# Kernel optimization log

Hardware: AMD Instinct MI355X
Metric: run time of the kernel (lower is better)

Reference implementation:

```python
import jax, jax.numpy as jnp
import numpy as np

V, D, H, KVH, HD, I, L, T_MAX, THETA = 32000, 1024, 16, 4, 64, 2816, 2, 2048, 10000.0
EPS = 1e-5


def rmsnorm(x, w):
    return x * jax.lax.rsqrt(jnp.mean(x * x, axis=-1, keepdims=True) + EPS) * w


def rope_cos_sin(T):
    inv = 1.0 / (THETA ** (jnp.arange(0, HD, 2, dtype=jnp.float32) / HD))  # [HD/2]
    ang = jnp.arange(T, dtype=jnp.float32)[:, None] * inv[None, :]         # [T, HD/2]
    return jnp.cos(ang), jnp.sin(ang)


def apply_rope(x, cos, sin):
    # x: [B, T, h, HD]; interleaved complex pairs as in torch.view_as_complex
    x0 = x[..., 0::2]
    x1 = x[..., 1::2]
    c = cos[None, :, None, :]
    s = sin[None, :, None, :]
    o0 = x0 * c - x1 * s
    o1 = x0 * s + x1 * c
    return jnp.stack([o0, o1], axis=-1).reshape(x.shape)


def setup_inputs() -> dict:
    key = jax.random.key(0)
    ks = jax.random.split(key, 12)
    sc = 0.02
    return {
        "toks": jax.random.randint(ks[0], (1, 2048), 0, V),
        "embed": jax.random.normal(ks[1], (V, D), jnp.float32) * sc,
        "Wq": jax.random.normal(ks[2], (L, D, H * HD), jnp.float32) * sc,
        "Wk": jax.random.normal(ks[3], (L, D, KVH * HD), jnp.float32) * sc,
        "Wv": jax.random.normal(ks[4], (L, D, KVH * HD), jnp.float32) * sc,
        "Wo": jax.random.normal(ks[5], (L, H * HD, D), jnp.float32) * sc,
        "Wgate": jax.random.normal(ks[6], (L, D, I), jnp.float32) * sc,
        "Wup": jax.random.normal(ks[7], (L, D, I), jnp.float32) * sc,
        "Wdown": jax.random.normal(ks[8], (L, I, D), jnp.float32) * sc,
        "ln1_w": jnp.ones((L, D), jnp.float32),
        "ln2_w": jnp.ones((L, D), jnp.float32),
        "norm_w": jnp.ones((D,), jnp.float32),
        "Wlm": jax.random.normal(ks[9], (D, V), jnp.float32) * sc,
    }


def reference(toks, embed, Wq, Wk, Wv, Wo, Wgate, Wup, Wdown, ln1_w, ln2_w, norm_w, Wlm):
    B, T = toks.shape
    cos, sin = rope_cos_sin(T)
    causal = jnp.tril(jnp.ones((T, T), dtype=bool))
    add_mask = jnp.where(causal, 0.0, -jnp.inf).astype(jnp.float32)  # [T, T]
    n_rep = H // KVH
    scale = 1.0 / np.sqrt(HD)

    x = embed[toks]  # [B, T, D]
    for l in range(L):
        h = rmsnorm(x, ln1_w[l])
        q = (h @ Wq[l]).reshape(B, T, H, HD)
        k = (h @ Wk[l]).reshape(B, T, KVH, HD)
        v = (h @ Wv[l]).reshape(B, T, KVH, HD)
        q = apply_rope(q, cos, sin)
        k = apply_rope(k, cos, sin)
        k = jnp.repeat(k, n_rep, axis=2)  # GQA repeat_kv -> [B, T, H, HD]
        v = jnp.repeat(v, n_rep, axis=2)
        # materialized scores [B, H, T, T] (faithful to source)
        scores = jnp.einsum('bqhd,bkhd->bhqk', q, k) * scale + add_mask[None, None]
        probs = jax.nn.softmax(scores, axis=-1)
        attn = jnp.einsum('bhqk,bkhd->bqhd', probs, v).reshape(B, T, H * HD)
        x = x + attn @ Wo[l]
        h = rmsnorm(x, ln2_w[l])
        x = x + (jax.nn.silu(h @ Wgate[l]) * (h @ Wup[l])) @ Wdown[l]

    x = rmsnorm(x, norm_w)
    return x @ Wlm  # [B, T, V]
```

## Files before the change

### kernel.cpp

```cpp
#include <hip/hip_runtime.h>

#define T_SEQ 2048
#define DMODEL 1024
#define NH 16
#define NKV 4
#define HEAD_DIM 64
#define FFDIM 2816
#define NVOCAB 32000

#define QBLK 64
#define KBLK 128
#define KSS 72
#define VTS 136
#define PSS 136

using u16 = unsigned short;
typedef __bf16 bf16x8 __attribute__((ext_vector_type(8)));
typedef float f32x4 __attribute__((ext_vector_type(4)));

__device__ __forceinline__ float b2f(u16 u) {
    union { unsigned int i; float f; } v; v.i = ((unsigned int)u) << 16; return v.f;
}
__device__ __forceinline__ u16 f2b(float f) {
    unsigned int u = __builtin_bit_cast(unsigned int, f);
    unsigned int r = (u + 0x7FFFu + ((u >> 16) & 1u)) >> 16;
    return (u16)r;
}
__device__ __forceinline__ void gload16(const u16* g, u16* l) {
    __builtin_amdgcn_global_load_lds(
        (const __attribute__((address_space(1))) void*)g,
        (__attribute__((address_space(3))) void*)l, 16, 0, 0);
}

__global__ __launch_bounds__(256) void embed_kernel(const int* __restrict__ toks,
                                                    const float* __restrict__ emb,
                                                    float* __restrict__ x) {
    int idx = blockIdx.x * 256 + threadIdx.x;
    int t = idx >> 10, d = idx & 1023;
    x[idx] = emb[(size_t)toks[t] * DMODEL + d];
}

__global__ __launch_bounds__(256) void rmsnorm_kernel(const float* __restrict__ x,
                                                      const float* __restrict__ w,
                                                      u16* __restrict__ out) {
    __shared__ float red[256];
    const int row = blockIdx.x, tid = threadIdx.x;
    const float* xr = x + (size_t)row * DMODEL;
    float vals[4]; float ss = 0.f;
#pragma unroll
    for (int i = 0; i < 4; i++) { float v = xr[tid + 256 * i]; vals[i] = v; ss += v * v; }
    red[tid] = ss; __syncthreads();
    for (int s = 128; s > 0; s >>= 1) { if (tid < s) red[tid] += red[tid + s]; __syncthreads(); }
    float inv = rsqrtf(red[0] * (1.0f / DMODEL) + 1e-5f);
#pragma unroll
    for (int i = 0; i < 4; i++) {
        int c = tid + 256 * i;
        out[(size_t)row * DMODEL + c] = f2b(vals[i] * inv * w[c]);
    }
}

__global__ __launch_bounds__(256) void tcast_kernel(const float* __restrict__ in,
                                                    u16* __restrict__ out, int K, int N) {
    __shared__ float tile[32][33];
    int bx = blockIdx.x * 32;
    int by = blockIdx.y * 32;
    int tx = threadIdx.x & 31, ty = threadIdx.x >> 5;
#pragma unroll
    for (int i = 0; i < 32; i += 8)
        tile[ty + i][tx] = in[(size_t)(by + ty + i) * N + bx + tx];
    __syncthreads();
#pragma unroll
    for (int i = 0; i < 32; i += 8)
        out[(size_t)(bx + ty + i) * K + by + tx] = f2b(tile[tx][ty + i]);
}

__global__ __launch_bounds__(256) void vtcast_kernel(const float* __restrict__ fqkv,
                                                     u16* __restrict__ vt) {
    __shared__ float tile[32][33];
    int bx = blockIdx.x * 32;
    int by = blockIdx.y * 32;
    int tx = threadIdx.x & 31, ty = threadIdx.x >> 5;
#pragma unroll
    for (int i = 0; i < 32; i += 8)
        tile[ty + i][tx] = fqkv[(size_t)(by + ty + i) * 1536 + 1280 + bx + tx];
    __syncthreads();
#pragma unroll
    for (int i = 0; i < 32; i += 8)
        vt[(size_t)(bx + ty + i) * T_SEQ + by + tx] = f2b(tile[tx][ty + i]);
}

__global__ __launch_bounds__(256) void gemm_bt_kernel(const u16* __restrict__ A,
                                                      const u16* __restrict__ BT,
                                                      float* __restrict__ C,
                                                      int N, int K) {
    __shared__ __align__(16) u16 As[128 * 32];
    __shared__ __align__(16) u16 Bs[128 * 32];
    const int tid = threadIdx.x;
    const int brow = blockIdx.x, bcol = blockIdx.y;
    const int w = tid >> 6, lane = tid & 63;
    const int wr = w >> 1, wc = w & 1;
    const int lg = lane >> 4, lr = lane & 15;

    f32x4 acc[4][4] = {};

    const int srow = w * 32 + (lane >> 2);
    const int scol = (lane & 3) << 3;
    const u16* gA = A + (size_t)(brow * 128 + srow) * K + scol;
    const u16* gB = BT + (size_t)(bcol * 128 + srow) * K + scol;
    u16* lA0 = &As[(w * 32) * 32];
    u16* lA1 = &As[(w * 32 + 16) * 32];
    u16* lB0 = &Bs[(w * 32) * 32];
    u16* lB1 = &Bs[(w * 32 + 16) * 32];

    for (int kb = 0; kb < K; kb += 32) {
        gload16(gA + kb, lA0);
        gload16(gA + (size_t)16 * K + kb, lA1);
        gload16(gB + kb, lB0);
        gload16(gB + (size_t)16 * K + kb, lB1);
        __syncthreads();

        bf16x8 aF[4], bF[4];
#pragma unroll
        for (int m = 0; m < 4; m++)
            aF[m] = *(const bf16x8*)(&As[(wr * 64 + m * 16 + lr) * 32 + lg * 8]);
#pragma unroll
        for (int n = 0; n < 4; n++)
            bF[n] = *(const bf16x8*)(&Bs[(wc * 64 + n * 16 + lr) * 32 + lg * 8]);
#pragma unroll
        for (int m = 0; m < 4; m++)
#pragma unroll
            for (int n = 0; n < 4; n++)
                acc[m][n] = __builtin_amdgcn_mfma_f32_16x16x32_bf16(aF[m], bF[n], acc[m][n], 0, 0, 0);
        __syncthreads();
    }

#pragma unroll
    for (int m = 0; m < 4; m++)
#pragma unroll
        for (int n = 0; n < 4; n++)
#pragma unroll
            for (int j = 0; j < 4; j++) {
                int row = brow * 128 + wr * 64 + m * 16 + lg * 4 + j;
                int col = bcol * 128 + wc * 64 + n * 16 + lr;
                C[(size_t)row * N + col] = acc[m][n][j];
            }
}

__device__ __forceinline__ int bs_off(int c, int k) {
    return c * 40 + ((((k >> 3) ^ ((c >> 3) & 3)) << 3) | (k & 7));
}

__global__ __launch_bounds__(256) void gemm_f32b_kernel(const u16* __restrict__ A,
                                                        const float* __restrict__ B,
                                                        float* __restrict__ C,
                                                        int N, int K) {
    __shared__ __align__(16) u16 As[128 * 40];
    __shared__ __align__(16) u16 Bs[128 * 40];
    const int tid = threadIdx.x;
    const int brow = blockIdx.y, bcol = blockIdx.x;
    const int wid = tid >> 6, lane = tid & 63;
    const int wr = wid >> 1, wc = wid & 1;
    const int lg = lane >> 4, lr = lane & 15;

    f32x4 acc[4][4] = {};
    const int ar = tid >> 2, ac = (tid & 3) << 3;
    const int bk = tid >> 4, bc = (tid & 15) << 3;

    for (int kb = 0; kb < K; kb += 32) {
        {
            const u16* ga = A + (size_t)(brow * 128 + ar) * K + kb + ac;
            *(uint4*)(&As[ar * 40 + ac]) = *(const uint4*)ga;
            *(uint4*)(&As[(ar + 64) * 40 + ac]) = *(const uint4*)(ga + (size_t)64 * K);
        }
        {
            const float* gb = B + (size_t)(kb + bk) * N + bcol * 128 + bc;
            float4 a0 = *(const float4*)gb;
            float4 a1 = *(const float4*)(gb + 4);
            float4 b0 = *(const float4*)(gb + (size_t)16 * N);
            float4 b1 = *(const float4*)(gb + (size_t)16 * N + 4);
            float f0[8] = {a0.x, a0.y, a0.z, a0.w, a1.x, a1.y, a1.z, a1.w};
            float f1[8] = {b0.x, b0.y, b0.z, b0.w, b1.x, b1.y, b1.z, b1.w};
#pragma unroll
            for (int i = 0; i < 8; i++) {
                Bs[bs_off(bc + i, bk)] = f2b(f0[i]);
                Bs[bs_off(bc + i, bk + 16)] = f2b(f1[i]);
            }
        }
        __syncthreads();

        bf16x8 aF[4], bF[4];
#pragma unroll
        for (int m = 0; m < 4; m++)
            aF[m] = *(const bf16x8*)(&As[(wr * 64 + m * 16 + lr) * 40 + lg * 8]);
#pragma unroll
        for (int n = 0; n < 4; n++) {
            int c = wc * 64 + n * 16 + lr;
            bF[n] = *(const bf16x8*)(&Bs[c * 40 + ((lg ^ ((c >> 3) & 3)) << 3)]);
        }
#pragma unroll
        for (int m = 0; m < 4; m++)
#pragma unroll
            for (int n = 0; n < 4; n++)
                acc[m][n] = __builtin_amdgcn_mfma_f32_16x16x32_bf16(aF[m], bF[n], acc[m][n], 0, 0, 0);
        __syncthreads();
    }

#pragma unroll
    for (int m = 0; m < 4; m++)
#pragma unroll
        for (int n = 0; n < 4; n++)
#pragma unroll
            for (int j = 0; j < 4; j++) {
                int row = brow * 128 + wr * 64 + m * 16 + lg * 4 + j;
                int col = bcol * 128 + wc * 64 + n * 16 + lr;
                C[(size_t)row * N + col] = acc[m][n][j];
            }
}

__global__ __launch_bounds__(256) void rope_kernel(const float* __restrict__ in,
                                                   u16* __restrict__ out, int heads,
                                                   int instride, int incoloff) {
    int idx = blockIdx.x * 256 + threadIdx.x;
    int total = T_SEQ * heads * 32;
    if (idx >= total) return;
    int i = idx & 31;
    int rest = idx >> 5;
    int t = rest / heads, hh = rest - t * heads;
    float inv = expf(-(float)i * (9.210340371976184f / 32.0f));
    float ang = (float)t * inv;
    float c = cosf(ang), s = sinf(ang);
    size_t src = (size_t)t * instride + incoloff + hh * HEAD_DIM + 2 * i;
    size_t dst = (size_t)rest * HEAD_DIM + 2 * i;
    float x0 = in[src], x1 = in[src + 1];
    out[dst]     = f2b(x0 * c - x1 * s);
    out[dst + 1] = f2b(x0 * s + x1 * c);
}

__global__ __launch_bounds__(256) void fattn_kernel(const u16* __restrict__ q,
                                                    const u16* __restrict__ k,
                                                    const u16* __restrict__ vt,
                                                    u16* __restrict__ out) {
    __shared__ __align__(16) u16 Ks[KBLK * KSS];
    __shared__ __align__(16) u16 Vt[HEAD_DIM * VTS];
    __shared__ __align__(16) u16 Ps[QBLK * PSS];
    const int tid = threadIdx.x;
    const int qb0 = blockIdx.x * QBLK, h = blockIdx.y, kvh = h >> 2;
    const int w = tid >> 6, lane = tid & 63;
    const int lg = lane >> 4, lr = lane & 15;

    bf16x8 qf0, qf1;
    {
        const u16* src = q + ((size_t)(qb0 + w * 16 + lr) * NH + h) * HEAD_DIM;
        qf0 = *(const bf16x8*)(src + lg * 8);
        qf1 = *(const bf16x8*)(src + 32 + lg * 8);
    }

    f32x4 acc_o[4] = {};
    float m_run[4] = {-1e30f, -1e30f, -1e30f, -1e30f};
    float l_run[4] = {0.f, 0.f, 0.f, 0.f};

    const int ntiles = (qb0 + QBLK - 1) / KBLK + 1;

    for (int kt = 0; kt < ntiles; kt++) {
        const int kb = kt * KBLK;
        __syncthreads();
        for (int c = tid; c < KBLK * 8; c += 256) {
            int row = c >> 3, c8 = (c & 7) << 3;
            *(uint4*)(&Ks[row * KSS + c8]) =
                *(const uint4*)(k + ((size_t)(kb + row) * NKV + kvh) * HEAD_DIM + c8);
        }
        for (int c = tid; c < HEAD_DIM * 16; c += 256) {
            int d = c >> 4, c16 = (c & 15) << 3;
            *(uint4*)(&Vt[d * VTS + c16]) =
                *(const uint4*)(vt + (size_t)(kvh * HEAD_DIM + d) * T_SEQ + kb + c16);
        }
        __syncthreads();

        f32x4 s[8] = {};
#pragma unroll
        for (int n = 0; n < 8; n++) {
            bf16x8 kf0 = *(const bf16x8*)(&Ks[(n * 16 + lr) * KSS + lg * 8]);
            bf16x8 kf1 = *(const bf16x8*)(&Ks[(n * 16 + lr) * KSS + 32 + lg * 8]);
            s[n] = __builtin_amdgcn_mfma_f32_16x16x32_bf16(qf0, kf0, s[n], 0, 0, 0);
            s[n] = __builtin_amdgcn_mfma_f32_16x16x32_bf16(qf1, kf1, s[n], 0, 0, 0);
        }

#pragma unroll
        for (int j = 0; j < 4; j++) {
            int q_g = qb0 + w * 16 + lg * 4 + j;
            float sv[8];
            float tmax = -1e30f;
#pragma unroll
            for (int n = 0; n < 8; n++) {
                float xx = s[n][j] * 0.125f;
                if (kb + n * 16 + lr > q_g) xx = -1e30f;
                sv[n] = xx;
                tmax = fmaxf(tmax, xx);
            }
#pragma unroll
            for (int mm = 1; mm < 16; mm <<= 1) tmax = fmaxf(tmax, __shfl_xor(tmax, mm));
            float mn = fmaxf(m_run[j], tmax);
            float sc = __expf(m_run[j] - mn);
            m_run[j] = mn;
            float rsum = 0.f;
#pragma unroll
            for (int n = 0; n < 8; n++) {
                float p = __expf(sv[n] - mn);
                rsum += p;
                Ps[(w * 16 + lg * 4 + j) * PSS + n * 16 + lr] = f2b(p);
            }
#pragma unroll
            for (int mm = 1; mm < 16; mm <<= 1) rsum += __shfl_xor(rsum, mm);
            l_run[j] = l_run[j] * sc + rsum;
#pragma unroll
            for (int n = 0; n < 4; n++) acc_o[n][j] *= sc;
        }

#pragma unroll
        for (int ks = 0; ks < 4; ks++) {
            bf16x8 pf = *(const bf16x8*)(&Ps[(w * 16 + lr) * PSS + ks * 32 + lg * 8]);
#pragma unroll
            for (int n = 0; n < 4; n++) {
                bf16x8 vf = *(const bf16x8*)(&Vt[(n * 16 + lr) * VTS + ks * 32 + lg * 8]);
                acc_o[n] = __builtin_amdgcn_mfma_f32_16x16x32_bf16(pf, vf, acc_o[n], 0, 0, 0);
            }
        }
    }

#pragma unroll
    for (int n = 0; n < 4; n++)
#pragma unroll
        for (int j = 0; j < 4; j++) {
            int t = qb0 + w * 16 + lg * 4 + j;
            int d = n * 16 + lr;
            out[((size_t)t * NH + h) * HEAD_DIM + d] = f2b(acc_o[n][j] / l_run[j]);
        }
}

__global__ __launch_bounds__(256) void silu_mul_kernel(const float* __restrict__ gu,
                                                       u16* __restrict__ out) {
    int t = blockIdx.x;
    int c = blockIdx.y * 256 + threadIdx.x;
    float gv = gu[(size_t)t * 5632 + c];
    float uv = gu[(size_t)t * 5632 + 2816 + c];
    float s = gv / (1.f + __expf(-gv));
    out[(size_t)t * FFDIM + c] = f2b(s * uv);
}

__global__ __launch_bounds__(256) void add_kernel(float* __restrict__ x,
                                                  const float* __restrict__ y, int n) {
    int i = blockIdx.x * 256 + threadIdx.x;
    if (i < n) x[i] += y[i];
}

extern "C" void kernel_launch(void* const* d_in, const int* in_sizes, int n_in,
                              void* d_out, int out_size, void* d_ws, size_t ws_size,
                              hipStream_t stream) {
    const int*   toks = (const int*)d_in[0];
    const float* emb  = (const float*)d_in[1];
    const float* Wq   = (const float*)d_in[2];
    const float* Wk   = (const float*)d_in[3];
    const float* Wv   = (const float*)d_in[4];
    const float* Wo   = (const float*)d_in[5];
    const float* Wg   = (const float*)d_in[6];
    const float* Wu   = (const float*)d_in[7];
    const float* Wd   = (const float*)d_in[8];
    const float* ln1  = (const float*)d_in[9];
    const float* ln2  = (const float*)d_in[10];
    const float* nw   = (const float*)d_in[11];
    const float* Wlm  = (const float*)d_in[12];

    char* ob = (char*)d_out;
    const size_t MB = 1024 * 1024;
    float* x    = (float*)(ob + 0 * MB);
    float* fqkv = (float*)(ob + 8 * MB);
    float* fGU  = (float*)(ob + 20 * MB);
    float* fA   = (float*)(ob + 64 * MB);
    u16* vt     = (u16*)  (ob + 72 * MB);
    u16* qb     = (u16*)  (ob + 74 * MB);
    u16* kb     = (u16*)  (ob + 78 * MB);
    u16* attnb  = (u16*)  (ob + 80 * MB);
    u16* ffb    = (u16*)  (ob + 84 * MB);
    size_t woff = 96 * MB;
    auto walloc = [&](size_t elems) {
        u16* p = (u16*)(ob + woff);
        woff += ((elems * 2 + 255) & ~(size_t)255);
        return p;
    };
    u16 *WqkvT[2], *WoT[2], *WguT[2], *WdT[2];
    for (int l = 0; l < 2; l++) {
        WqkvT[l] = walloc((size_t)1536 * DMODEL);
        WoT[l]   = walloc((size_t)DMODEL * DMODEL);
        WguT[l]  = walloc((size_t)5632 * DMODEL);
        WdT[l]   = walloc((size_t)DMODEL * FFDIM);
    }
    u16* h = (u16*)d_ws;
    bool ws_big = ws_size >= 72 * MB;
    u16* WlmT = ws_big ? (u16*)((char*)d_ws + 4 * MB) : nullptr;
    (void)in_sizes; (void)n_in; (void)out_size;

    dim3 blk(256);
    auto tcast = [&](const float* in, u16* out, int K, int N) {
        tcast_kernel<<<dim3(N / 32, K / 32), blk, 0, stream>>>(in, out, K, N);
    };
    auto gemm_bt = [&](const u16* A, const u16* BT, float* C, int N, int K) {
        dim3 g(T_SEQ / 128, N / 128);
        gemm_bt_kernel<<<g, blk, 0, stream>>>(A, BT, C, N, K);
    };

    for (int l = 0; l < 2; l++) {
        tcast(Wq + (size_t)l * DMODEL * NH * HEAD_DIM,  WqkvT[l],                    DMODEL, NH * HEAD_DIM);
        tcast(Wk + (size_t)l * DMODEL * NKV * HEAD_DIM, WqkvT[l] + (size_t)1024 * DMODEL, DMODEL, NKV * HEAD_DIM);
        tcast(Wv + (size_t)l * DMODEL * NKV * HEAD_DIM, WqkvT[l] + (size_t)1280 * DMODEL, DMODEL, NKV * HEAD_DIM);
        tcast(Wo + (size_t)l * DMODEL * DMODEL,         WoT[l],  DMODEL, DMODEL);
        tcast(Wg + (size_t)l * DMODEL * FFDIM,          WguT[l],                     DMODEL, FFDIM);
        tcast(Wu + (size_t)l * DMODEL * FFDIM,          WguT[l] + (size_t)FFDIM * DMODEL, DMODEL, FFDIM);
        tcast(Wd + (size_t)l * FFDIM * DMODEL,          WdT[l],  FFDIM, DMODEL);
    }
    if (WlmT) tcast(Wlm, WlmT, DMODEL, NVOCAB);

    embed_kernel<<<dim3(T_SEQ * DMODEL / 256), blk, 0, stream>>>(toks, emb, x);

    for (int l = 0; l < 2; l++) {
        rmsnorm_kernel<<<dim3(T_SEQ), blk, 0, stream>>>(x, ln1 + (size_t)l * DMODEL, h);
        gemm_bt(h, WqkvT[l], fqkv, 1536, DMODEL);
        rope_kernel<<<dim3(T_SEQ * NH * 32 / 256), blk, 0, stream>>>(fqkv, qb, NH, 1536, 0);
        rope_kernel<<<dim3(T_SEQ * NKV * 32 / 256), blk, 0, stream>>>(fqkv, kb, NKV, 1536, 1024);
        vtcast_kernel<<<dim3(8, T_SEQ / 32), blk, 0, stream>>>(fqkv, vt);
        fattn_kernel<<<dim3(T_SEQ / QBLK, NH), blk, 0, stream>>>(qb, kb, vt, attnb);
        gemm_bt(attnb, WoT[l], fA, DMODEL, DMODEL);
        add_kernel<<<dim3(T_SEQ * DMODEL / 256), blk, 0, stream>>>(x, fA, T_SEQ * DMODEL);

        rmsnorm_kernel<<<dim3(T_SEQ), blk, 0, stream>>>(x, ln2 + (size_t)l * DMODEL, h);
        gemm_bt(h, WguT[l], fGU, 5632, DMODEL);
        silu_mul_kernel<<<dim3(T_SEQ, FFDIM / 256), blk, 0, stream>>>(fGU, ffb);
        gemm_bt(ffb, WdT[l], fA, DMODEL, FFDIM);
        add_kernel<<<dim3(T_SEQ * DMODEL / 256), blk, 0, stream>>>(x, fA, T_SEQ * DMODEL);
    }

    rmsnorm_kernel<<<dim3(T_SEQ), blk, 0, stream>>>(x, nw, h);
    if (WlmT) {
        gemm_bt(h, WlmT, (float*)d_out, NVOCAB, DMODEL);
    } else {
        dim3 g(NVOCAB / 128, T_SEQ / 128);
        gemm_f32b_kernel<<<g, blk, 0, stream>>>(h, Wlm, (float*)d_out, NVOCAB, DMODEL);
    }
}
```

Before: 906.9 us.

## Double-buffer LDS tiles and remap workgroups across XCDs in bf16 GEMM

Converts the GEMM K-loop to double-buffered LDS so the next tile's global-to-LDS load is issued before computing on the current tile, leaving one barrier per iteration. Also remaps the linear workgroup id so consecutive tiles run on the same XCD, improving L2 reuse of A/B rows. This doubles LDS use per block, which may lower occupancy, and relies on the async loads finishing before the single barrier.

```diff
diff --git a/kernel.cpp b/kernel.cpp
--- a/kernel.cpp
+++ b/kernel.cpp
@@ -93,10 +93,17 @@
                                                       const u16* __restrict__ BT,
                                                       float* __restrict__ C,
                                                       int N, int K) {
-    __shared__ __align__(16) u16 As[128 * 32];
-    __shared__ __align__(16) u16 Bs[128 * 32];
+    __shared__ __align__(16) u16 As[2][128 * 32];
+    __shared__ __align__(16) u16 Bs[2][128 * 32];
     const int tid = threadIdx.x;
-    const int brow = blockIdx.x, bcol = blockIdx.y;
+    const int gx = gridDim.x;
+    const int nwg = gx * gridDim.y;
+    const int hwid = blockIdx.y * gx + blockIdx.x;
+    const int q = nwg >> 3, r = nwg & 7;
+    const int xcd = hwid & 7, rem = hwid >> 3;
+    const int wgid = (xcd < r ? xcd * (q + 1) : r * (q + 1) + (xcd - r) * q) + rem;
+    const int brow = wgid % gx, bcol = wgid / gx;
+
     const int w = tid >> 6, lane = tid & 63;
     const int wr = w >> 1, wc = w & 1;
     const int lg = lane >> 4, lr = lane & 15;
@@ -107,31 +114,39 @@
     const int scol = (lane & 3) << 3;
     const u16* gA = A + (size_t)(brow * 128 + srow) * K + scol;
     const u16* gB = BT + (size_t)(bcol * 128 + srow) * K + scol;
-    u16* lA0 = &As[(w * 32) * 32];
-    u16* lA1 = &As[(w * 32 + 16) * 32];
-    u16* lB0 = &Bs[(w * 32) * 32];
-    u16* lB1 = &Bs[(w * 32 + 16) * 32];
-
-    for (int kb = 0; kb < K; kb += 32) {
-        gload16(gA + kb, lA0);
-        gload16(gA + (size_t)16 * K + kb, lA1);
-        gload16(gB + kb, lB0);
-        gload16(gB + (size_t)16 * K + kb, lB1);
-        __syncthreads();
-
+    const int lofs0 = (w * 32) * 32;
+    const int lofs1 = (w * 32 + 16) * 32;
+
+    const int nt = K >> 5;
+    gload16(gA, &As[0][lofs0]);
+    gload16(gA + (size_t)16 * K, &As[0][lofs1]);
+    gload16(gB, &Bs[0][lofs0]);
+    gload16(gB + (size_t)16 * K, &Bs[0][lofs1]);
+    __syncthreads();
+
+    int cur = 0;
+    for (int t = 0; t < nt; t++) {
+        if (t + 1 < nt) {
+            const int kb = (t + 1) << 5;
+            gload16(gA + kb, &As[cur ^ 1][lofs0]);
+            gload16(gA + (size_t)16 * K + kb, &As[cur ^ 1][lofs1]);
+            gload16(gB + kb, &Bs[cur ^ 1][lofs0]);
+            gload16(gB + (size_t)16 * K + kb, &Bs[cur ^ 1][lofs1]);
+        }
         bf16x8 aF[4], bF[4];
 #pragma unroll
         for (int m = 0; m < 4; m++)
-            aF[m] = *(const bf16x8*)(&As[(wr * 64 + m * 16 + lr) * 32 + lg * 8]);
+            aF[m] = *(const bf16x8*)(&As[cur][(wr * 64 + m * 16 + lr) * 32 + lg * 8]);
 #pragma unroll
         for (int n = 0; n < 4; n++)
-            bF[n] = *(const bf16x8*)(&Bs[(wc * 64 + n * 16 + lr) * 32 + lg * 8]);
+            bF[n] = *(const bf16x8*)(&Bs[cur][(wc * 64 + n * 16 + lr) * 32 + lg * 8]);
 #pragma unroll
         for (int m = 0; m < 4; m++)
 #pragma unroll
             for (int n = 0; n < 4; n++)
                 acc[m][n] = __builtin_amdgcn_mfma_f32_16x16x32_bf16(aF[m], bF[n], acc[m][n], 0, 0, 0);
         __syncthreads();
+        cur ^= 1;
     }
 
 #pragma unroll
```

Result: faster. 851.1 us (-6.2%).
